# Kernel optimization log

Hardware: AMD Instinct MI355X
Metric: run time of the kernel (lower is better)

## Reference

```python
import jax, jax.numpy as jnp
import numpy as np

B = 32768
D_A, D_V, D_T = 512, 512, 768
D_KW, D_CTX, D_SPK = 256, 256, 128
H = 512
IN_A = D_V + D_T + D_KW + D_CTX + D_SPK  # 1920 = visual + other_dim (text+hidden+speaker)
IN_V = D_A + D_T + D_KW + D_CTX + D_SPK  # 1920


def _linear_params(key, din, dout):
    kw, kb = jax.random.split(key)
    bound = 1.0 / np.sqrt(din)
    W = jax.random.uniform(kw, (din, dout), jnp.float32, -bound, bound)
    b = jax.random.uniform(kb, (dout,), jnp.float32, -bound, bound)
    return W, b


def setup_inputs() -> dict:
    key = jax.random.key(0)
    ks = jax.random.split(key, 16)
    inp = {
        'audio': jax.random.normal(ks[0], (B, D_A), jnp.float32),
        'visual': jax.random.normal(ks[1], (B, D_V), jnp.float32),
        'text': jax.random.normal(ks[2], (B, D_T), jnp.float32),
        'keywords': jax.random.normal(ks[3], (B, D_KW), jnp.float32),
        'context': jax.random.normal(ks[4], (B, D_CTX), jnp.float32),
        'speaker_embed': jax.random.normal(ks[5], (B, D_SPK), jnp.float32),
    }
    # Masks restricted to dimensionally-consistent patterns: [0,1,1] or [1,0,1]
    r = jax.random.randint(ks[6], (B,), 0, 2)
    inp['modality_masks'] = jnp.stack([r, 1 - r, jnp.ones_like(r)], axis=1).astype(jnp.int32)
    # audio_imagination MLP params
    inp['aW1'], inp['ab1'] = _linear_params(ks[7], IN_A, H)
    inp['aW2'], inp['ab2'] = _linear_params(ks[8], H, H)
    inp['aW3'], inp['ab3'] = _linear_params(ks[9], H, D_A)
    # visual_imagination MLP params
    inp['vW1'], inp['vb1'] = _linear_params(ks[10], IN_V, H)
    inp['vW2'], inp['vb2'] = _linear_params(ks[11], H, H)
    inp['vW3'], inp['vb3'] = _linear_params(ks[12], H, D_V)
    return inp


def _mlp(x, W1, b1, W2, b2, W3, b3):
    h = jax.nn.relu(x @ W1 + b1)  # dropout is eval-mode identity
    h = jax.nn.relu(h @ W2 + b2)
    return h @ W3 + b3


def reference(audio, visual, text, keywords, context, speaker_embed, modality_masks,
              aW1, ab1, aW2, ab2, aW3, ab3,
              vW1, vb1, vW2, vb2, vW3, vb3):
    m = modality_masks.astype(audio.dtype)
    common = jnp.concatenate([keywords, context, speaker_embed], axis=-1)  # [B, 640]
    in_a = jnp.concatenate([visual, text, common], axis=-1)  # [B, IN_A]
    in_v = jnp.concatenate([audio, text, common], axis=-1)   # [B, IN_V]
    # Rows where the modality is present (mask==1) were omitted in the original
    # ragged stacking; here they are zeroed to keep a fixed [B, D] output.
    recon_audio = _mlp(in_a, aW1, ab1, aW2, ab2, aW3, ab3) * (1.0 - m[:, 0:1])
    recon_visual = _mlp(in_v, vW1, vb1, vW2, vb2, vW3, vb3) * (1.0 - m[:, 1:2])
    return recon_audio, recon_visual
```

## Files before the change

### kernel.cpp

```cpp
#include <hip/hip_runtime.h>
#include <stdint.h>

typedef __bf16 bf16;
typedef __bf16 bf16x8 __attribute__((ext_vector_type(8)));
typedef float  f32x4  __attribute__((ext_vector_type(4)));

#define NROWS 32768
#define HID   512

__device__ __forceinline__ void gload_lds16(const void* g, void* l) {
  __builtin_amdgcn_global_load_lds(
      (const __attribute__((address_space(1))) void*)g,
      (__attribute__((address_space(3))) void*)l, 16, 0, 0);
}

__global__ void prep_transpose(const float* __restrict__ W, bf16* __restrict__ WT,
                               int K, int N) {
  __shared__ float t[32][33];
  int k0 = blockIdx.x * 32, n0 = blockIdx.y * 32;
  int tx = threadIdx.x, ty = threadIdx.y;
#pragma unroll
  for (int p = 0; p < 4; ++p)
    t[ty + p * 8][tx] = W[(size_t)(k0 + ty + p * 8) * N + n0 + tx];
  __syncthreads();
#pragma unroll
  for (int p = 0; p < 4; ++p) {
    int n = n0 + ty + p * 8;
    int k = k0 + tx;
    int ks = (k & ~63) | (((((k >> 3) & 7) ^ (n & 7))) << 3) | (k & 7);
    WT[(size_t)n * K + ks] = (bf16)t[tx][ty + p * 8];
  }
}

__global__ void count_rows(const int* __restrict__ masks, int* __restrict__ bcnt) {
  int i = blockIdx.x * 256 + threadIdx.x;
  int lane = threadIdx.x & 63, wv = threadIdx.x >> 6;
  unsigned long long vA = __ballot(masks[i * 3] == 0);
  __shared__ int c[4];
  if (lane == 0) c[wv] = __popcll(vA);
  __syncthreads();
  if (threadIdx.x == 0) bcnt[blockIdx.x] = c[0] + c[1] + c[2] + c[3];
}

__global__ void scan_blocks(const int* __restrict__ bcnt, int* __restrict__ baseA,
                            int* __restrict__ counts) {
  __shared__ int s[128];
  s[threadIdx.x] = bcnt[threadIdx.x];
  __syncthreads();
  if (threadIdx.x == 0) {
    int run = 0;
    for (int i = 0; i < 128; ++i) { int v = s[i]; s[i] = run; run += v; }
    counts[0] = run; counts[1] = NROWS - run;
  }
  __syncthreads();
  baseA[threadIdx.x] = s[threadIdx.x];
}

__global__ void write_idx(const int* __restrict__ masks, const int* __restrict__ baseA,
                          int* __restrict__ idxA, int* __restrict__ idxV) {
  int b = blockIdx.x, t = threadIdx.x, i = b * 256 + t;
  int lane = t & 63, wv = t >> 6;
  int r = masks[i * 3];
  unsigned long long vA = __ballot(r == 0);
  __shared__ int wc[4];
  if (lane == 0) wc[wv] = __popcll(vA);
  __syncthreads();
  int wA = 0;
#pragma unroll
  for (int w = 0; w < 4; ++w) if (w < wv) wA += wc[w];
  unsigned long long ltmask = (lane == 63) ? (~0ULL >> 1) : ((1ULL << lane) - 1);
  int posA = __popcll(vA & ltmask);
  int bA = baseA[b];
  if (r == 0) idxA[bA + wA + posA] = i;
  else        idxV[(256 * b - bA) + (64 * wv - wA) + (lane - posA)] = i;
}

template <int LAYER>
__global__ __launch_bounds__(512, 4) void mlp_gemm(
    const float* __restrict__ audio, const float* __restrict__ visual,
    const float* __restrict__ text,  const float* __restrict__ kwd,
    const float* __restrict__ ctx,   const float* __restrict__ spk,
    const bf16*  __restrict__ hin,
    const bf16*  __restrict__ WTa,   const bf16* __restrict__ WTv,
    const float* __restrict__ ba,    const float* __restrict__ bv,
    const int*   __restrict__ counts,
    const int*   __restrict__ idxA,  const int* __restrict__ idxV,
    bf16* __restrict__ hout, float* __restrict__ out) {
  constexpr int K = (LAYER == 1) ? 1920 : 512;
  constexpr int NT = K / 64;
  const int mlp = blockIdx.z;
  const int cnt = counts[mlp];
  const int m0 = blockIdx.x * 128;
  if (m0 >= cnt) return;
  const int n0 = blockIdx.y * 128;
  const bf16*  WT   = mlp ? WTv : WTa;
  const float* bias = mlp ? bv : ba;
  const int*   idx  = mlp ? idxV : idxA;

  __shared__ __attribute__((aligned(16))) bf16 sA[2][128 * 64];
  __shared__ __attribute__((aligned(16))) bf16 sB[2][128 * 64];

  const int t = threadIdx.x;
  const int lane = t & 63;
  const int wave = t >> 6;
  const int wm = (wave >> 1) * 32;
  const int wn = (wave & 1) * 64;

  int gidx[2];
  if constexpr (LAYER == 1) {
#pragma unroll
    for (int rep = 0; rep < 2; ++rep) {
      int row = (t + rep * 512) >> 3;
      int i = m0 + row;
      if (i >= cnt) i = cnt - 1;
      gidx[rep] = idx[i];
    }
  }

  f32x4 pa[2], pb[2];

  auto B_ISSUE = [&](int k0, int buf) {
#pragma unroll
    for (int rep = 0; rep < 2; ++rep) {
      int sbase = rep * 512 + wave * 64;
      int slot = sbase + lane;
      int row = slot >> 3, wc = slot & 7;
      gload_lds16(WT + (size_t)(n0 + row) * K + k0 + wc * 8, &sB[buf][sbase * 8]);
    }
  };
  auto A_ISSUE_LDS = [&](int k0, int buf) {
#pragma unroll
    for (int rep = 0; rep < 2; ++rep) {
      int sbase = rep * 512 + wave * 64;
      int slot = sbase + lane;
      int row = slot >> 3, wc = slot & 7;
      gload_lds16(hin + ((size_t)mlp * NROWS + m0 + row) * HID + k0 + wc * 8,
                  &sA[buf][sbase * 8]);
    }
  };
  auto A_ISSUE = [&](int k0) {
    const float* seg; int soff, sstr;
    if (k0 < 512)       { seg = mlp ? audio : visual; soff = k0;        sstr = 512; }
    else if (k0 < 1280) { seg = text; soff = k0 - 512;  sstr = 768; }
    else if (k0 < 1536) { seg = kwd;  soff = k0 - 1280; sstr = 256; }
    else if (k0 < 1792) { seg = ctx;  soff = k0 - 1536; sstr = 256; }
    else                { seg = spk;  soff = k0 - 1792; sstr = 128; }
#pragma unroll
    for (int rep = 0; rep < 2; ++rep) {
      int slot = t + rep * 512;
      int c = slot & 7;
      const float* src = seg + (size_t)gidx[rep] * sstr + soff + c * 8;
      pa[rep] = *(const f32x4*)src;
      pb[rep] = *(const f32x4*)(src + 4);
    }
  };
  auto A_WRITE = [&](int buf) {
#pragma unroll
    for (int rep = 0; rep < 2; ++rep) {
      int slot = t + rep * 512;
      int row = slot >> 3, c = slot & 7;
      int wc = c ^ (row & 7);
      bf16x8 v;
      v[0] = (bf16)pa[rep][0]; v[1] = (bf16)pa[rep][1];
      v[2] = (bf16)pa[rep][2]; v[3] = (bf16)pa[rep][3];
      v[4] = (bf16)pb[rep][0]; v[5] = (bf16)pb[rep][1];
      v[6] = (bf16)pb[rep][2]; v[7] = (bf16)pb[rep][3];
      *(bf16x8*)&sA[buf][row * 64 + wc * 8] = v;
    }
  };

  const f32x4 fzero = {0.f, 0.f, 0.f, 0.f};
  f32x4 acc[2][4];
#pragma unroll
  for (int a = 0; a < 2; ++a)
#pragma unroll
    for (int b = 0; b < 4; ++b) acc[a][b] = fzero;

  if constexpr (LAYER == 1) { A_ISSUE(0); A_WRITE(0); }
  else                      { A_ISSUE_LDS(0, 0); }
  B_ISSUE(0, 0);
  __syncthreads();

  int cur = 0;
  for (int ti = 0; ti < NT; ++ti) {
    const int k0 = ti * 64;
    const bool pf = (ti + 1 < NT);
    if (pf) {
      if constexpr (LAYER == 1) A_ISSUE(k0 + 64);
      else                      A_ISSUE_LDS(k0 + 64, cur ^ 1);
      B_ISSUE(k0 + 64, cur ^ 1);
    }
    bf16x8 af[2][2], bfr[4][2];
#pragma unroll
    for (int mf = 0; mf < 2; ++mf)
#pragma unroll
      for (int kh = 0; kh < 2; ++kh) {
        int row = wm + mf * 16 + (lane & 15);
        int c = (lane >> 4) + kh * 4;
        af[mf][kh] = *(const bf16x8*)&sA[cur][row * 64 + (c ^ (row & 7)) * 8];
      }
#pragma unroll
    for (int nf = 0; nf < 4; ++nf)
#pragma unroll
      for (int kh = 0; kh < 2; ++kh) {
        int row = wn + nf * 16 + (lane & 15);
        int c = (lane >> 4) + kh * 4;
        bfr[nf][kh] = *(const bf16x8*)&sB[cur][row * 64 + (c ^ (row & 7)) * 8];
      }
#pragma unroll
    for (int mf = 0; mf < 2; ++mf)
#pragma unroll
      for (int nf = 0; nf < 4; ++nf)
#pragma unroll
        for (int kh = 0; kh < 2; ++kh)
          acc[mf][nf] = __builtin_amdgcn_mfma_f32_16x16x32_bf16(
              af[mf][kh], bfr[nf][kh], acc[mf][nf], 0, 0, 0);
    if constexpr (LAYER == 1) {
      if (pf) A_WRITE(cur ^ 1);
    }
    __syncthreads();
    cur ^= 1;
  }

  const int r4 = (lane >> 4) * 4;
  const int cl = lane & 15;
#pragma unroll
  for (int mf = 0; mf < 2; ++mf) {
#pragma unroll
    for (int reg = 0; reg < 4; ++reg) {
      int lrow = wm + mf * 16 + r4 + reg;
      int grow = m0 + lrow;
      if (grow >= cnt) continue;
      if constexpr (LAYER < 3) {
#pragma unroll
        for (int nf = 0; nf < 4; ++nf) {
          int col = n0 + wn + nf * 16 + cl;
          float v = acc[mf][nf][reg] + bias[col];
          v = fmaxf(v, 0.f);
          int cs = (col & ~63) | (((((col >> 3) & 7) ^ (grow & 7))) << 3) | (col & 7);
          hout[((size_t)mlp * NROWS + grow) * HID + cs] = (bf16)v;
        }
      } else {
        int g = idx[grow];
#pragma unroll
        for (int nf = 0; nf < 4; ++nf) {
          int col = n0 + wn + nf * 16 + cl;
          float v = acc[mf][nf][reg] + bias[col];
          out[((size_t)mlp * NROWS + g) * 512 + col] = v;
          out[((size_t)(1 - mlp) * NROWS + g) * 512 + col] = 0.f;
        }
      }
    }
  }
}

extern "C" void kernel_launch(void* const* d_in, const int* in_sizes, int n_in,
                              void* d_out, int out_size, void* d_ws, size_t ws_size,
                              hipStream_t stream) {
  (void)in_sizes; (void)n_in; (void)out_size;
  const float* audio  = (const float*)d_in[0];
  const float* visual = (const float*)d_in[1];
  const float* text   = (const float*)d_in[2];
  const float* kwd    = (const float*)d_in[3];
  const float* ctx    = (const float*)d_in[4];
  const float* spk    = (const float*)d_in[5];
  const int*   masks  = (const int*)d_in[6];
  const float* aW1 = (const float*)d_in[7];  const float* ab1 = (const float*)d_in[8];
  const float* aW2 = (const float*)d_in[9];  const float* ab2 = (const float*)d_in[10];
  const float* aW3 = (const float*)d_in[11]; const float* ab3 = (const float*)d_in[12];
  const float* vW1 = (const float*)d_in[13]; const float* vb1 = (const float*)d_in[14];
  const float* vW2 = (const float*)d_in[15]; const float* vb2 = (const float*)d_in[16];
  const float* vW3 = (const float*)d_in[17]; const float* vb3 = (const float*)d_in[18];
  float* out = (float*)d_out;

  char* w = (char*)d_ws;
  int* counts = (int*)w;
  int* bcnt   = (int*)(w + 256);
  int* baseA  = (int*)(w + 1024);
  int* idxA = (int*)(w + 4096);
  int* idxV = idxA + 32768;
  bf16* aW1t = (bf16*)(w + 4096 + 262144);
  bf16* vW1t = aW1t + 983040;
  bf16* aW2t = vW1t + 983040;
  bf16* vW2t = aW2t + 262144;
  bf16* aW3t = vW2t + 262144;
  bf16* vW3t = aW3t + 262144;
  bf16* h1 = vW3t + 262144;
  bf16* h2 = h1 + (size_t)2 * NROWS * HID;
  (void)ws_size;

  count_rows<<<128, 256, 0, stream>>>(masks, bcnt);
  scan_blocks<<<1, 128, 0, stream>>>(bcnt, baseA, counts);
  write_idx<<<128, 256, 0, stream>>>(masks, baseA, idxA, idxV);

  dim3 tb(32, 8);
  prep_transpose<<<dim3(60, 16), tb, 0, stream>>>(aW1, aW1t, 1920, 512);
  prep_transpose<<<dim3(60, 16), tb, 0, stream>>>(vW1, vW1t, 1920, 512);
  prep_transpose<<<dim3(16, 16), tb, 0, stream>>>(aW2, aW2t, 512, 512);
  prep_transpose<<<dim3(16, 16), tb, 0, stream>>>(vW2, vW2t, 512, 512);
  prep_transpose<<<dim3(16, 16), tb, 0, stream>>>(aW3, aW3t, 512, 512);
  prep_transpose<<<dim3(16, 16), tb, 0, stream>>>(vW3, vW3t, 512, 512);

  dim3 gg(136, 4, 2);
  mlp_gemm<1><<<gg, 512, 0, stream>>>(audio, visual, text, kwd, ctx, spk, nullptr,
                                      aW1t, vW1t, ab1, vb1, counts, idxA, idxV, h1, nullptr);
  mlp_gemm<2><<<gg, 512, 0, stream>>>(audio, visual, text, kwd, ctx, spk, h1,
                                      aW2t, vW2t, ab2, vb2, counts, idxA, idxV, h2, nullptr);
  mlp_gemm<3><<<gg, 512, 0, stream>>>(audio, visual, text, kwd, ctx, spk, h2,
                                      aW3t, vW3t, ab3, vb3, counts, idxA, idxV, nullptr, out);
}
```

Baseline: 256.2 us.

## Enlarge GEMM tiles to 128x256 with triple-buffered phased pipeline

Doubles the N tile to 256 so each wave computes a 64x64 output, and replaces the double-buffered loop with a three-stage LDS ring. Each k-step is split into four phases that interleave global loads, LDS reads and MFMA bursts, using explicit waitcnt, barriers and s_setprio. The M-block order is remapped, and the hidden buffers are resized to a padded row count of 17408. The aim is more operand reuse per tile and better hiding of load latency. In exchange, LDS and register use rise and occupancy drops to one block per SIMD group, and the hand-tuned waitcnt counts could go wrong if the load counts change.

Result: slower. 297.7 us (+16.2%).

```diff
diff --git a/kernel.cpp b/kernel.cpp
--- a/kernel.cpp
+++ b/kernel.cpp
@@ -7,6 +7,7 @@
 
 #define NROWS 32768
 #define HID   512
+#define PADM  17408
 
 __device__ __forceinline__ void gload_lds16(const void* g, void* l) {
   __builtin_amdgcn_global_load_lds(
@@ -76,7 +77,7 @@
 }
 
 template <int LAYER>
-__global__ __launch_bounds__(512, 4) void mlp_gemm(
+__global__ __launch_bounds__(512, 1) void mlp_gemm(
     const float* __restrict__ audio, const float* __restrict__ visual,
     const float* __restrict__ text,  const float* __restrict__ kwd,
     const float* __restrict__ ctx,   const float* __restrict__ spk,
@@ -90,21 +91,22 @@
   constexpr int NT = K / 64;
   const int mlp = blockIdx.z;
   const int cnt = counts[mlp];
-  const int m0 = blockIdx.x * 128;
+  const int mb = (blockIdx.x & 7) * 17 + (blockIdx.x >> 3);
+  const int m0 = mb * 128;
   if (m0 >= cnt) return;
-  const int n0 = blockIdx.y * 128;
+  const int n0 = blockIdx.y * 256;
   const bf16*  WT   = mlp ? WTv : WTa;
   const float* bias = mlp ? bv : ba;
   const int*   idx  = mlp ? idxV : idxA;
 
-  __shared__ __attribute__((aligned(16))) bf16 sA[2][128 * 64];
-  __shared__ __attribute__((aligned(16))) bf16 sB[2][128 * 64];
+  __shared__ __attribute__((aligned(16))) bf16 sA[3][128 * 64];
+  __shared__ __attribute__((aligned(16))) bf16 sB[3][256 * 64];
 
   const int t = threadIdx.x;
   const int lane = t & 63;
   const int wave = t >> 6;
-  const int wm = (wave >> 1) * 32;
-  const int wn = (wave & 1) * 64;
+  const int wm = (wave >> 2) * 64;
+  const int wn = (wave & 3) * 64;
 
   int gidx[2];
   if constexpr (LAYER == 1) {
@@ -119,26 +121,29 @@
 
   f32x4 pa[2], pb[2];
 
-  auto B_ISSUE = [&](int k0, int buf) {
-#pragma unroll
-    for (int rep = 0; rep < 2; ++rep) {
-      int sbase = rep * 512 + wave * 64;
+  auto B_STAGE = [&](int ti) {
+    const int k0 = ti * 64, buf = ti % 3;
+#pragma unroll
+    for (int r = 0; r < 4; ++r) {
+      int sbase = r * 512 + wave * 64;
       int slot = sbase + lane;
       int row = slot >> 3, wc = slot & 7;
       gload_lds16(WT + (size_t)(n0 + row) * K + k0 + wc * 8, &sB[buf][sbase * 8]);
     }
   };
-  auto A_ISSUE_LDS = [&](int k0, int buf) {
-#pragma unroll
-    for (int rep = 0; rep < 2; ++rep) {
-      int sbase = rep * 512 + wave * 64;
+  auto A_STAGE_G = [&](int ti) {
+    const int k0 = ti * 64, buf = ti % 3;
+#pragma unroll
+    for (int r = 0; r < 2; ++r) {
+      int sbase = r * 512 + wave * 64;
       int slot = sbase + lane;
       int row = slot >> 3, wc = slot & 7;
-      gload_lds16(hin + ((size_t)mlp * NROWS + m0 + row) * HID + k0 + wc * 8,
+      gload_lds16(hin + ((size_t)mlp * PADM + m0 + row) * HID + k0 + wc * 8,
                   &sA[buf][sbase * 8]);
     }
   };
-  auto A_ISSUE = [&](int k0) {
+  auto A_LOADS = [&](int ti) {
+    const int k0 = ti * 64;
     const float* seg; int soff, sstr;
     if (k0 < 512)       { seg = mlp ? audio : visual; soff = k0;        sstr = 512; }
     else if (k0 < 1280) { seg = text; soff = k0 - 512;  sstr = 768; }
@@ -154,7 +159,8 @@
       pb[rep] = *(const f32x4*)(src + 4);
     }
   };
-  auto A_WRITE = [&](int buf) {
+  auto A_CVTWR = [&](int ti) {
+    const int buf = ti % 3;
 #pragma unroll
     for (int rep = 0; rep < 2; ++rep) {
       int slot = t + rep * 512;
@@ -170,62 +176,96 @@
   };
 
   const f32x4 fzero = {0.f, 0.f, 0.f, 0.f};
-  f32x4 acc[2][4];
-#pragma unroll
-  for (int a = 0; a < 2; ++a)
+  f32x4 acc[4][4];
+#pragma unroll
+  for (int a = 0; a < 4; ++a)
 #pragma unroll
     for (int b = 0; b < 4; ++b) acc[a][b] = fzero;
 
-  if constexpr (LAYER == 1) { A_ISSUE(0); A_WRITE(0); }
-  else                      { A_ISSUE_LDS(0, 0); }
-  B_ISSUE(0, 0);
-  __syncthreads();
-
-  int cur = 0;
+  if constexpr (LAYER == 1) {
+    A_LOADS(0);
+    A_CVTWR(0);
+    A_LOADS(1);
+    B_STAGE(0);
+    asm volatile("s_waitcnt vmcnt(4)" ::: "memory");
+    __builtin_amdgcn_sched_barrier(0);
+    A_CVTWR(1);
+    B_STAGE(1);
+    asm volatile("s_waitcnt vmcnt(4) lgkmcnt(0)" ::: "memory");
+  } else {
+    A_STAGE_G(0); B_STAGE(0);
+    A_STAGE_G(1); B_STAGE(1);
+    asm volatile("s_waitcnt vmcnt(6)" ::: "memory");
+  }
+  __builtin_amdgcn_sched_barrier(0);
+  __builtin_amdgcn_s_barrier();
+
+#define PHASE(KH, MH, STAGE_CODE, TAIL_WAIT_CODE)                              \
+  {                                                                            \
+    bf16x8 af[2], bv4[4];                                                      \
+    _Pragma("unroll")                                                          \
+    for (int mi = 0; mi < 2; ++mi) {                                           \
+      int row = wm + ((MH)*2 + mi) * 16 + (lane & 15);                         \
+      int c = (lane >> 4) + (KH)*4;                                            \
+      af[mi] = *(const bf16x8*)&sA[bufc][row * 64 + (c ^ (row & 7)) * 8];      \
+    }                                                                          \
+    _Pragma("unroll")                                                          \
+    for (int nf = 0; nf < 4; ++nf) {                                           \
+      int row = wn + nf * 16 + (lane & 15);                                    \
+      int c = (lane >> 4) + (KH)*4;                                            \
+      bv4[nf] = *(const bf16x8*)&sB[bufc][row * 64 + (c ^ (row & 7)) * 8];     \
+    }                                                                          \
+    STAGE_CODE;                                                                \
+    __builtin_amdgcn_s_barrier();                                              \
+    asm volatile("s_waitcnt lgkmcnt(0)" ::: "memory");                         \
+    __builtin_amdgcn_sched_barrier(0);                                         \
+    __builtin_amdgcn_s_setprio(1);                                             \
+    _Pragma("unroll")                                                          \
+    for (int mi = 0; mi < 2; ++mi)                                             \
+      _Pragma("unroll")                                                        \
+      for (int nf = 0; nf < 4; ++nf)                                           \
+        acc[(MH)*2 + mi][nf] = __builtin_amdgcn_mfma_f32_16x16x32_bf16(        \
+            af[mi], bv4[nf], acc[(MH)*2 + mi][nf], 0, 0, 0);                   \
+    __builtin_amdgcn_s_setprio(0);                                             \
+    __builtin_amdgcn_sched_barrier(0);                                         \
+    TAIL_WAIT_CODE;                                                            \
+    __builtin_amdgcn_s_barrier();                                              \
+  }
+
   for (int ti = 0; ti < NT; ++ti) {
-    const int k0 = ti * 64;
-    const bool pf = (ti + 1 < NT);
-    if (pf) {
-      if constexpr (LAYER == 1) A_ISSUE(k0 + 64);
-      else                      A_ISSUE_LDS(k0 + 64, cur ^ 1);
-      B_ISSUE(k0 + 64, cur ^ 1);
-    }
-    bf16x8 af[2][2], bfr[4][2];
-#pragma unroll
-    for (int mf = 0; mf < 2; ++mf)
-#pragma unroll
-      for (int kh = 0; kh < 2; ++kh) {
-        int row = wm + mf * 16 + (lane & 15);
-        int c = (lane >> 4) + kh * 4;
-        af[mf][kh] = *(const bf16x8*)&sA[cur][row * 64 + (c ^ (row & 7)) * 8];
-      }
-#pragma unroll
-    for (int nf = 0; nf < 4; ++nf)
-#pragma unroll
-      for (int kh = 0; kh < 2; ++kh) {
-        int row = wn + nf * 16 + (lane & 15);
-        int c = (lane >> 4) + kh * 4;
-        bfr[nf][kh] = *(const bf16x8*)&sB[cur][row * 64 + (c ^ (row & 7)) * 8];
-      }
-#pragma unroll
-    for (int mf = 0; mf < 2; ++mf)
-#pragma unroll
-      for (int nf = 0; nf < 4; ++nf)
-#pragma unroll
-        for (int kh = 0; kh < 2; ++kh)
-          acc[mf][nf] = __builtin_amdgcn_mfma_f32_16x16x32_bf16(
-              af[mf][kh], bfr[nf][kh], acc[mf][nf], 0, 0, 0);
+    const int bufc = ti % 3;
+    const int tc = (ti + 2 < NT) ? (ti + 2) : (NT - 1);
+
     if constexpr (LAYER == 1) {
-      if (pf) A_WRITE(cur ^ 1);
-    }
-    __syncthreads();
-    cur ^= 1;
-  }
+      PHASE(0, 0, { A_LOADS(tc); }, {});
+    } else {
+      PHASE(0, 0, { A_STAGE_G(tc); }, {});
+    }
+    PHASE(0, 1, { B_STAGE(tc); }, {});
+    if constexpr (LAYER == 1) {
+      PHASE(1, 0,
+            {
+              asm volatile("s_waitcnt vmcnt(4)" ::: "memory");
+              __builtin_amdgcn_sched_barrier(0);
+              A_CVTWR(tc);
+            },
+            {});
+    } else {
+      PHASE(1, 0, {}, {});
+    }
+    if constexpr (LAYER == 1) {
+      PHASE(1, 1, {}, { asm volatile("s_waitcnt vmcnt(4)" ::: "memory"); });
+    } else {
+      PHASE(1, 1, {}, { asm volatile("s_waitcnt vmcnt(6)" ::: "memory"); });
+    }
+  }
+#undef PHASE
+  asm volatile("s_waitcnt vmcnt(0) lgkmcnt(0)" ::: "memory");
 
   const int r4 = (lane >> 4) * 4;
   const int cl = lane & 15;
 #pragma unroll
-  for (int mf = 0; mf < 2; ++mf) {
+  for (int mf = 0; mf < 4; ++mf) {
 #pragma unroll
     for (int reg = 0; reg < 4; ++reg) {
       int lrow = wm + mf * 16 + r4 + reg;
@@ -238,7 +278,7 @@
           float v = acc[mf][nf][reg] + bias[col];
           v = fmaxf(v, 0.f);
           int cs = (col & ~63) | (((((col >> 3) & 7) ^ (grow & 7))) << 3) | (col & 7);
-          hout[((size_t)mlp * NROWS + grow) * HID + cs] = (bf16)v;
+          hout[((size_t)mlp * PADM + grow) * HID + cs] = (bf16)v;
         }
       } else {
         int g = idx[grow];
@@ -286,7 +326,7 @@
   bf16* aW3t = vW2t + 262144;
   bf16* vW3t = aW3t + 262144;
   bf16* h1 = vW3t + 262144;
-  bf16* h2 = h1 + (size_t)2 * NROWS * HID;
+  bf16* h2 = h1 + (size_t)2 * PADM * HID;
   (void)ws_size;
 
   count_rows<<<128, 256, 0, stream>>>(masks, bcnt);
@@ -301,7 +341,7 @@
   prep_transpose<<<dim3(16, 16), tb, 0, stream>>>(aW3, aW3t, 512, 512);
   prep_transpose<<<dim3(16, 16), tb, 0, stream>>>(vW3, vW3t, 512, 512);
 
-  dim3 gg(136, 4, 2);
+  dim3 gg(136, 2, 2);
   mlp_gemm<1><<<gg, 512, 0, stream>>>(audio, visual, text, kwd, ctx, spk, nullptr,
                                       aW1t, vW1t, ab1, vb1, counts, idxA, idxV, h1, nullptr);
   mlp_gemm<2><<<gg, 512, 0, stream>>>(audio, visual, text, kwd, ctx, spk, h1,
```
